# Performance work log

Hardware: AMD Instinct MI355X
Metric: run time of the kernel (lower is better)

The kernel has to match this reference:

```python
import jax, jax.numpy as jnp
import numpy as np

N_DOF = 7
WIDTH = 1024
BATCH = 8192
EPS = 1e-5
LSIZE = N_DOF * (N_DOF + 1) // 2   # diag (n) + strictly-lower ((n^2-n)/2)


def _tri_idx(n):
    # order matches LowTri: offset -i chunks, within-chunk j -> entry (j+i, j)
    r, c = [], []
    for i in range(n):
        for j in range(n - i):
            r.append(j + i)
            c.append(j)
    return np.array(r, np.int32), np.array(c, np.int32)

_R, _C = _tri_idx(N_DOF)


def setup_inputs() -> dict:
    key = jax.random.key(0)
    ks = jax.random.split(key, 9)

    def glorot(k, shape):
        std = (2.0 / (shape[0] + shape[1])) ** 0.5
        return (jax.random.normal(k, shape, jnp.float32) * std).astype(jnp.float32)

    lower = LSIZE - N_DOF
    b0 = 0.1
    return {
        "state": jax.random.normal(ks[0], (BATCH, N_DOF), jnp.float32),
        "velocity": jax.random.normal(ks[1], (BATCH, N_DOF), jnp.float32),
        "acceleration": jax.random.normal(ks[2], (BATCH, N_DOF), jnp.float32),
        "W_in": glorot(ks[3], (N_DOF, WIDTH)), "b_in": jnp.full((WIDTH,), b0, jnp.float32),
        "W_h": glorot(ks[4], (WIDTH, WIDTH)), "b_h": jnp.full((WIDTH,), b0, jnp.float32),
        "W_g": glorot(ks[5], (WIDTH, 1)), "b_g": jnp.full((1,), b0, jnp.float32),
        "W_ld": glorot(ks[6], (WIDTH, N_DOF)), "b_ld": jnp.full((N_DOF,), b0, jnp.float32),
        "W_lo": glorot(ks[7], (WIDTH, lower)), "b_lo": jnp.full((lower,), b0, jnp.float32),
    }


def _layer(x, der, W, b, act):
    # a: [B, out]; der: [B, in, n_dof] -> [B, out, n_dof]
    a = x @ W + b
    if act == "relu":
        y = jax.nn.relu(a)
        gp = (a > 0).astype(a.dtype)
    else:  # linear
        y = a
        gp = jnp.ones_like(a)
    # diag(g'(a)) @ W^T @ prev_der  ==  g'(a)[:, :, None] * (W^T @ prev_der)
    new_der = gp[:, :, None] * jnp.einsum("io,bid->bod", W, der)
    return y, new_der


def _forward(state, velocity, acceleration,
             W_in, b_in, W_h, b_h, W_g, b_g, W_ld, b_ld, W_lo, b_lo):
    B = state.shape[0]
    eye = jnp.broadcast_to(jnp.eye(N_DOF, dtype=state.dtype), (B, N_DOF, N_DOF))

    y1, d1 = _layer(state, eye, W_in, b_in, "relu")
    y2, d2 = _layer(y1, d1, W_h, b_h, "relu")
    y3, d3 = _layer(y2, d2, W_h, b_h, "relu")   # original reuses hidden_layer1 twice

    V, derV = _layer(y3, d3, W_g, b_g, "linear")       # derV: [B, 1, n_dof]
    l_diag, der_ld = _layer(y3, d3, W_ld, b_ld, "relu")
    l_low, der_lo = _layer(y3, d3, W_lo, b_lo, "linear")

    l = jnp.concatenate([l_diag, l_low], axis=1)          # [B, LSIZE]
    der_l = jnp.concatenate([der_ld, der_lo], axis=1)     # [B, LSIZE, n_dof]

    def lowtri(v):   # [B, LSIZE] -> [B, n, n]
        return jnp.zeros((B, N_DOF, N_DOF), v.dtype).at[:, _R, _C].set(v)

    def lowtri3d(v):  # [B, n_dof, LSIZE] -> [B, n_dof, n, n]
        return jnp.zeros((B, N_DOF, N_DOF, N_DOF), v.dtype).at[:, :, _R, _C].set(v)

    L = lowtri(l)
    LT = jnp.swapaxes(L, 1, 2)
    M = L @ LT + EPS * jnp.eye(N_DOF, dtype=L.dtype)

    dldt = jnp.einsum("bld,bd->bl", der_l, velocity)
    dLdt = lowtri(dldt)
    dMdt = L @ jnp.swapaxes(dLdt, 1, 2) + dLdt @ LT

    dLdq = lowtri3d(jnp.swapaxes(der_l, 1, 2))            # [B, n_dof, n, n]
    dMdq = dLdq @ LT[:, None] + L[:, None] @ jnp.swapaxes(dLdq, 2, 3)

    dMdt_dq = jnp.einsum("bij,bj->bi", dMdt, velocity)
    quad_dq = jnp.einsum("bi,bkij,bj->bk", velocity, dMdq, velocity)
    C = dMdt_dq - 0.5 * quad_dq
    G = derV[:, 0, :]                                      # squeeze [B,1,n_dof]
    Mddq = jnp.einsum("bij,bj->bi", M, acceleration)
    tau_pred = Mddq + C + G
    return tau_pred, M, C, G


def reference(state, velocity, acceleration,
              W_in, b_in, W_h, b_h, W_g, b_g, W_ld, b_ld, W_lo, b_lo):
    return _forward(state, velocity, acceleration,
                    W_in, b_in, W_h, b_h, W_g, b_g, W_ld, b_ld, W_lo, b_lo)
```

## Files before the change

### kernel.cpp

```cpp
#include <hip/hip_runtime.h>
#include <hip/hip_bf16.h>

#define WIDTH 1024
#define BATCH 8192

typedef __attribute__((ext_vector_type(8))) short short8;
typedef __attribute__((ext_vector_type(4))) float floatx4;

typedef __attribute__((address_space(1))) void gvoid;
typedef __attribute__((address_space(3))) void lvoid;

__device__ __forceinline__ void async_copy16(const void* g, void* l) {
    __builtin_amdgcn_global_load_lds((gvoid*)g, (lvoid*)l, 16, 0, 0);
}

__device__ __forceinline__ void split_store(float v, __hip_bfloat16* hi, __hip_bfloat16* lo, long idx) {
    __hip_bfloat16 h = __float2bfloat16(v);
    hi[idx] = h;
    lo[idx] = __float2bfloat16(v - __bfloat162float(h));
}

__global__ __launch_bounds__(256) void transpose_k(
    const float* __restrict__ W,
    __hip_bfloat16* __restrict__ Wth, __hip_bfloat16* __restrict__ Wtl)
{
    __shared__ float t[32][33];
    const int tx = threadIdx.x & 31, ty = threadIdx.x >> 5;
    const int bx = blockIdx.x << 5, by = blockIdx.y << 5;
#pragma unroll
    for (int r = 0; r < 32; r += 8)
        t[ty + r][tx] = W[(long)(by + ty + r) * WIDTH + bx + tx];
    __syncthreads();
#pragma unroll
    for (int r = 0; r < 32; r += 8)
        split_store(t[tx][ty + r], Wth, Wtl, (long)(bx + ty + r) * WIDTH + by + tx);
}

__global__ __launch_bounds__(256) void buildwcat_k(
    const float* __restrict__ W_ld, const float* __restrict__ W_lo,
    const float* __restrict__ W_g,
    __hip_bfloat16* __restrict__ Wch, __hip_bfloat16* __restrict__ Wcl)
{
    const int idx = blockIdx.x * 256 + threadIdx.x;
    const int n = idx >> 10, k = idx & 1023;
    float v = 0.f;
    if (n < 7)       v = W_ld[k * 7 + n];
    else if (n < 28) v = W_lo[k * 21 + (n - 7)];
    else if (n == 28) v = W_g[k];
    split_store(v, Wch, Wcl, idx);
}

__global__ __launch_bounds__(256) void prep_k(
    const float* __restrict__ state,
    const float* __restrict__ W_in,
    const float* __restrict__ b_in,
    __hip_bfloat16* __restrict__ Y1h, __hip_bfloat16* __restrict__ Y1l,
    __hip_bfloat16* __restrict__ D1h)
{
    const int b = blockIdx.x;
    const int j0 = threadIdx.x * 4;
    float s[7];
#pragma unroll
    for (int d = 0; d < 7; ++d) s[d] = state[b * 7 + d];
    float a[4];
#pragma unroll
    for (int q = 0; q < 4; ++q) a[q] = b_in[j0 + q];
    float w[7][4];
#pragma unroll
    for (int d = 0; d < 7; ++d)
#pragma unroll
        for (int q = 0; q < 4; ++q) {
            w[d][q] = W_in[d * WIDTH + j0 + q];
            a[q] += s[d] * w[d][q];
        }
    bool gp[4];
#pragma unroll
    for (int q = 0; q < 4; ++q) {
        gp[q] = a[q] > 0.f;
        split_store(gp[q] ? a[q] : 0.f, Y1h, Y1l, (long)b * WIDTH + j0 + q);
    }
    union { unsigned long long u64; unsigned short h[4]; } pk;
#pragma unroll
    for (int d = 0; d < 7; ++d) {
#pragma unroll
        for (int q = 0; q < 4; ++q) {
            __hip_bfloat16 v = __float2bfloat16(gp[q] ? w[d][q] : 0.f);
            pk.h[q] = *reinterpret_cast<unsigned short*>(&v);
        }
        *reinterpret_cast<unsigned long long*>(&D1h[((long)b * 7 + d) * WIDTH + j0]) = pk.u64;
    }
}

__device__ __forceinline__ void y_gemm_body(
    short* SM,
    int bm, int bn, int tid,
    const __hip_bfloat16* Ah, const __hip_bfloat16* Al,
    const __hip_bfloat16* Bh, const __hip_bfloat16* Bl,
    const float* bias,
    __hip_bfloat16* outh, __hip_bfloat16* outl)
{
    short* Ash = SM;          short* Asl = SM + 4096;
    short* Bsh = SM + 8192;   short* Bsl = SM + 12288;
    const int lane = tid & 63;
    const int wv = tid >> 6;
    const int wm = wv >> 1, wn = wv & 1;
    const int srow = tid >> 2;
    const int scol = (tid & 3) << 3;
    const short* pAh = (const short*)Ah + (long)(bm * 128 + srow) * WIDTH + scol;
    const short* pAl = (const short*)Al + (long)(bm * 128 + srow) * WIDTH + scol;
    const short* pBh = (const short*)Bh + (long)(bn * 128 + srow) * WIDTH + scol;
    const short* pBl = (const short*)Bl + (long)(bn * 128 + srow) * WIDTH + scol;
    const long half = 64l * WIDTH;

    floatx4 acc[4][4] = {};
    const int r = lane & 15;
    const int kq = (lane >> 4) << 3;

    for (int kt = 0; kt < WIDTH; kt += 32) {
        __syncthreads();
        async_copy16(pAh + kt,        Ash + wv * 512);
        async_copy16(pAh + half + kt, Ash + 2048 + wv * 512);
        async_copy16(pAl + kt,        Asl + wv * 512);
        async_copy16(pAl + half + kt, Asl + 2048 + wv * 512);
        async_copy16(pBh + kt,        Bsh + wv * 512);
        async_copy16(pBh + half + kt, Bsh + 2048 + wv * 512);
        async_copy16(pBl + kt,        Bsl + wv * 512);
        async_copy16(pBl + half + kt, Bsl + 2048 + wv * 512);
        __syncthreads();
        short8 afh[4], afl[4], bfh[4], bfl[4];
#pragma unroll
        for (int i = 0; i < 4; ++i) {
            const int ar = (wm * 64 + i * 16 + r) * 32 + kq;
            afh[i] = *reinterpret_cast<const short8*>(&Ash[ar]);
            afl[i] = *reinterpret_cast<const short8*>(&Asl[ar]);
        }
#pragma unroll
        for (int j = 0; j < 4; ++j) {
            const int br = (wn * 64 + j * 16 + r) * 32 + kq;
            bfh[j] = *reinterpret_cast<const short8*>(&Bsh[br]);
            bfl[j] = *reinterpret_cast<const short8*>(&Bsl[br]);
        }
#pragma unroll
        for (int i = 0; i < 4; ++i)
#pragma unroll
            for (int j = 0; j < 4; ++j) {
                acc[i][j] = __builtin_amdgcn_mfma_f32_16x16x32_bf16(afh[i], bfh[j], acc[i][j], 0, 0, 0);
                acc[i][j] = __builtin_amdgcn_mfma_f32_16x16x32_bf16(afh[i], bfl[j], acc[i][j], 0, 0, 0);
                acc[i][j] = __builtin_amdgcn_mfma_f32_16x16x32_bf16(afl[i], bfh[j], acc[i][j], 0, 0, 0);
            }
    }

    const int r4 = (lane >> 4) << 2;
#pragma unroll
    for (int i = 0; i < 4; ++i)
#pragma unroll
        for (int j = 0; j < 4; ++j) {
            const int col = bn * 128 + wn * 64 + j * 16 + r;
#pragma unroll
            for (int rr = 0; rr < 4; ++rr) {
                const int row = bm * 128 + wm * 64 + i * 16 + r4 + rr;
                float v = acc[i][j][rr] + bias[col];
                v = v > 0.f ? v : 0.f;
                split_store(v, outh, outl, (long)row * WIDTH + col);
            }
        }
}

__global__ __launch_bounds__(256) void gemm_y(
    const __hip_bfloat16* __restrict__ Ah, const __hip_bfloat16* __restrict__ Al,
    const __hip_bfloat16* __restrict__ Bh, const __hip_bfloat16* __restrict__ Bl,
    const float* __restrict__ bias,
    __hip_bfloat16* __restrict__ outh, __hip_bfloat16* __restrict__ outl)
{
    __shared__ __align__(16) short SM[16384];
    y_gemm_body(SM, blockIdx.x, blockIdx.y, threadIdx.x, Ah, Al, Bh, Bl, bias, outh, outl);
}

__global__ __launch_bounds__(256) void d2y3_k(
    const __hip_bfloat16* __restrict__ D1,
    const __hip_bfloat16* __restrict__ Wth, const __hip_bfloat16* __restrict__ Wtl,
    const __hip_bfloat16* __restrict__ Y2h, const __hip_bfloat16* __restrict__ Y2l,
    const float* __restrict__ bias,
    __hip_bfloat16* __restrict__ D2out,
    __hip_bfloat16* __restrict__ Y3h, __hip_bfloat16* __restrict__ Y3l,
    int nd)
{
    __shared__ __align__(16) short SM[16384];
    const int tid = threadIdx.x;
    if ((int)blockIdx.x >= nd) {
        y_gemm_body(SM, blockIdx.x - nd, blockIdx.y, tid, Y2h, Y2l, Wth, Wtl, bias, Y3h, Y3l);
        return;
    }
    short* Ash0 = SM;         short* Ash1 = SM + 4096;
    short* Bsh0 = SM + 8192;  short* Bsh1 = SM + 12288;
    const int lane = tid & 63;
    const int wv = tid >> 6;
    const int wm = wv >> 1, wn = wv & 1;
    const int bm = blockIdx.x, bn = blockIdx.y;

    const int srow = tid >> 2;
    const int scol = (tid & 3) << 3;
    const short* pAh = (const short*)D1 + (long)(bm * 128 + srow) * WIDTH + scol;
    const short* pBh = (const short*)Wth + (long)(bn * 128 + srow) * WIDTH + scol;
    const long half = 64l * WIDTH;

    floatx4 acc[4][4] = {};
    const int r = lane & 15;
    const int kq = (lane >> 4) << 3;

    for (int kt = 0; kt < WIDTH; kt += 64) {
        __syncthreads();
        async_copy16(pAh + kt,             Ash0 + wv * 512);
        async_copy16(pAh + half + kt,      Ash0 + 2048 + wv * 512);
        async_copy16(pAh + kt + 32,        Ash1 + wv * 512);
        async_copy16(pAh + half + kt + 32, Ash1 + 2048 + wv * 512);
        async_copy16(pBh + kt,             Bsh0 + wv * 512);
        async_copy16(pBh + half + kt,      Bsh0 + 2048 + wv * 512);
        async_copy16(pBh + kt + 32,        Bsh1 + wv * 512);
        async_copy16(pBh + half + kt + 32, Bsh1 + 2048 + wv * 512);
        __syncthreads();
#pragma unroll
        for (int s = 0; s < 2; ++s) {
            const short* As = s ? Ash1 : Ash0;
            const short* Bs = s ? Bsh1 : Bsh0;
            short8 afh[4], bfh[4];
#pragma unroll
            for (int i = 0; i < 4; ++i)
                afh[i] = *reinterpret_cast<const short8*>(&As[(wm * 64 + i * 16 + r) * 32 + kq]);
#pragma unroll
            for (int j = 0; j < 4; ++j)
                bfh[j] = *reinterpret_cast<const short8*>(&Bs[(wn * 64 + j * 16 + r) * 32 + kq]);
#pragma unroll
            for (int i = 0; i < 4; ++i)
#pragma unroll
                for (int j = 0; j < 4; ++j)
                    acc[i][j] = __builtin_amdgcn_mfma_f32_16x16x32_bf16(afh[i], bfh[j], acc[i][j], 0, 0, 0);
        }
    }

    const int r4 = (lane >> 4) << 2;
#pragma unroll
    for (int i = 0; i < 4; ++i)
#pragma unroll
        for (int j = 0; j < 4; ++j) {
            const int col = bn * 128 + wn * 64 + j * 16 + r;
#pragma unroll
            for (int rr = 0; rr < 4; ++rr) {
                const int row = bm * 128 + wm * 64 + i * 16 + r4 + rr;
                float v = acc[i][j][rr];
                const unsigned brow = (unsigned)row / 7u;
                if (!(__bfloat162float(Y2h[(long)brow * WIDTH + col]) > 0.f)) v = 0.f;
                D2out[(long)row * WIDTH + col] = __float2bfloat16(v);
            }
        }
}

__global__ __launch_bounds__(256) void d3heady_k(
    const __hip_bfloat16* __restrict__ D2,
    const __hip_bfloat16* __restrict__ Wth, const __hip_bfloat16* __restrict__ Wtl,
    const __hip_bfloat16* __restrict__ Y3h, const __hip_bfloat16* __restrict__ Y3l,
    const __hip_bfloat16* __restrict__ Wch, const __hip_bfloat16* __restrict__ Wcl,
    float* __restrict__ PDpart, float* __restrict__ PY,
    int nd, int Mrows)
{
    __shared__ __align__(16) short SM[26112];
    const int tid = threadIdx.x;
    const int lane = tid & 63;
    const int wv = tid >> 6;
    const int r = lane & 15;
    const int kq = (lane >> 4) << 3;
    const int r4 = (lane >> 4) << 2;
    const int srow = tid >> 2;
    const int scol = (tid & 3) << 3;
    const long half = 64l * WIDTH;

    if ((int)blockIdx.x >= nd) {
        if (blockIdx.y != 0) return;
        short* Ash = SM;          short* Asl = SM + 4096;
        short* Bsh = SM + 8192;   short* Bsl = SM + 9216;
        const int bm = blockIdx.x - nd;
        const short* pAh = (const short*)Y3h + (long)(bm * 128 + srow) * WIDTH + scol;
        const short* pAl = (const short*)Y3l + (long)(bm * 128 + srow) * WIDTH + scol;
        const long boff = (long)srow * WIDTH + scol;
        const short* pBh = (const short*)Wch;  const short* pBl = (const short*)Wcl;

        floatx4 acc[2][2] = {};
        for (int kt = 0; kt < WIDTH; kt += 32) {
            short8 gbh, gbl;
            if (tid < 128) {
                gbh = *reinterpret_cast<const short8*>(pBh + boff + kt);
                gbl = *reinterpret_cast<const short8*>(pBl + boff + kt);
            }
            __syncthreads();
            async_copy16(pAh + kt,        Ash + wv * 512);
            async_copy16(pAh + half + kt, Ash + 2048 + wv * 512);
            async_copy16(pAl + kt,        Asl + wv * 512);
            async_copy16(pAl + half + kt, Asl + 2048 + wv * 512);
            if (tid < 128) {
                *reinterpret_cast<short8*>(&Bsh[srow * 32 + scol]) = gbh;
                *reinterpret_cast<short8*>(&Bsl[srow * 32 + scol]) = gbl;
            }
            __syncthreads();
            short8 afh[2], afl[2], bfh[2], bfl[2];
#pragma unroll
            for (int i = 0; i < 2; ++i) {
                const int ar = (wv * 32 + i * 16 + r) * 32 + kq;
                afh[i] = *reinterpret_cast<const short8*>(&Ash[ar]);
                afl[i] = *reinterpret_cast<const short8*>(&Asl[ar]);
            }
#pragma unroll
            for (int j = 0; j < 2; ++j) {
                const int br = (j * 16 + r) * 32 + kq;
                bfh[j] = *reinterpret_cast<const short8*>(&Bsh[br]);
                bfl[j] = *reinterpret_cast<const short8*>(&Bsl[br]);
            }
#pragma unroll
            for (int i = 0; i < 2; ++i)
#pragma unroll
                for (int j = 0; j < 2; ++j) {
                    acc[i][j] = __builtin_amdgcn_mfma_f32_16x16x32_bf16(afh[i], bfh[j], acc[i][j], 0, 0, 0);
                    acc[i][j] = __builtin_amdgcn_mfma_f32_16x16x32_bf16(afh[i], bfl[j], acc[i][j], 0, 0, 0);
                    acc[i][j] = __builtin_amdgcn_mfma_f32_16x16x32_bf16(afl[i], bfh[j], acc[i][j], 0, 0, 0);
                }
        }
#pragma unroll
        for (int i = 0; i < 2; ++i)
#pragma unroll
            for (int j = 0; j < 2; ++j)
#pragma unroll
                for (int rr = 0; rr < 4; ++rr) {
                    const int row = bm * 128 + wv * 32 + i * 16 + r4 + rr;
                    PY[(long)row * 32 + j * 16 + r] = acc[i][j][rr];
                }
        return;
    }

    short* Ash0 = SM;         short* Ash1 = SM + 4096;
    short* Bsh0 = SM + 8192;  short* Bsh1 = SM + 12288;
    short* T    = SM;
    short* WcH  = SM + 17408;
    short* WcL  = SM + 21760;

    const int wm = wv >> 1, wn = wv & 1;
    const int bm = blockIdx.x, bn = blockIdx.y;
    const short* pAh = (const short*)D2 + (long)(bm * 128 + srow) * WIDTH + scol;
    const short* pBh = (const short*)Wth + (long)(bn * 128 + srow) * WIDTH + scol;

    floatx4 acc[4][4] = {};
    for (int kt = 0; kt < WIDTH; kt += 64) {
        __syncthreads();
        async_copy16(pAh + kt,             Ash0 + wv * 512);
        async_copy16(pAh + half + kt,      Ash0 + 2048 + wv * 512);
        async_copy16(pAh + kt + 32,        Ash1 + wv * 512);
        async_copy16(pAh + half + kt + 32, Ash1 + 2048 + wv * 512);
        async_copy16(pBh + kt,             Bsh0 + wv * 512);
        async_copy16(pBh + half + kt,      Bsh0 + 2048 + wv * 512);
        async_copy16(pBh + kt + 32,        Bsh1 + wv * 512);
        async_copy16(pBh + half + kt + 32, Bsh1 + 2048 + wv * 512);
        __syncthreads();
#pragma unroll
        for (int s = 0; s < 2; ++s) {
            const short* As = s ? Ash1 : Ash0;
            const short* Bs = s ? Bsh1 : Bsh0;
            short8 afh[4], bfh[4];
#pragma unroll
            for (int i = 0; i < 4; ++i)
                afh[i] = *reinterpret_cast<const short8*>(&As[(wm * 64 + i * 16 + r) * 32 + kq]);
#pragma unroll
            for (int j = 0; j < 4; ++j)
                bfh[j] = *reinterpret_cast<const short8*>(&Bs[(wn * 64 + j * 16 + r) * 32 + kq]);
#pragma unroll
            for (int i = 0; i < 4; ++i)
#pragma unroll
                for (int j = 0; j < 4; ++j)
                    acc[i][j] = __builtin_amdgcn_mfma_f32_16x16x32_bf16(afh[i], bfh[j], acc[i][j], 0, 0, 0);
        }
    }

    __syncthreads();
#pragma unroll
    for (int i = 0; i < 4; ++i)
#pragma unroll
        for (int j = 0; j < 4; ++j) {
            const int coll = wn * 64 + j * 16 + r;
            const int colg = bn * 128 + coll;
#pragma unroll
            for (int rr = 0; rr < 4; ++rr) {
                const int rowl = wm * 64 + i * 16 + r4 + rr;
                const int rowg = bm * 128 + rowl;
                float v = acc[i][j][rr];
                const unsigned brow = (unsigned)rowg / 7u;
                if (!(__bfloat162float(Y3h[(long)brow * WIDTH + colg]) > 0.f)) v = 0.f;
                __hip_bfloat16 hb = __float2bfloat16(v);
                T[rowl * 136 + coll] = *reinterpret_cast<short*>(&hb);
            }
        }
    {
        const int n = tid >> 4, k8 = (tid & 15) * 8;
        const short* wh = (const short*)Wch;
        const short* wl = (const short*)Wcl;
        *reinterpret_cast<short8*>(&WcH[n * 136 + k8]) =
            *reinterpret_cast<const short8*>(wh + n * WIDTH + bn * 128 + k8);
        *reinterpret_cast<short8*>(&WcH[(n + 16) * 136 + k8]) =
            *reinterpret_cast<const short8*>(wh + (n + 16) * WIDTH + bn * 128 + k8);
        *reinterpret_cast<short8*>(&WcL[n * 136 + k8]) =
            *reinterpret_cast<const short8*>(wl + n * WIDTH + bn * 128 + k8);
        *reinterpret_cast<short8*>(&WcL[(n + 16) * 136 + k8]) =
            *reinterpret_cast<const short8*>(wl + (n + 16) * WIDTH + bn * 128 + k8);
    }
    __syncthreads();

    floatx4 accp[2][2] = {};
#pragma unroll
    for (int kk = 0; kk < 128; kk += 32) {
        short8 af[2], bh8[2], bl8[2];
#pragma unroll
        for (int i = 0; i < 2; ++i)
            af[i] = *reinterpret_cast<const short8*>(&T[(wv * 32 + i * 16 + r) * 136 + kk + kq]);
#pragma unroll
        for (int j = 0; j < 2; ++j) {
            bh8[j] = *reinterpret_cast<const short8*>(&WcH[(j * 16 + r) * 136 + kk + kq]);
            bl8[j] = *reinterpret_cast<const short8*>(&WcL[(j * 16 + r) * 136 + kk + kq]);
        }
#pragma unroll
        for (int i = 0; i < 2; ++i)
#pragma unroll
            for (int j = 0; j < 2; ++j) {
                accp[i][j] = __builtin_amdgcn_mfma_f32_16x16x32_bf16(af[i], bh8[j], accp[i][j], 0, 0, 0);
                accp[i][j] = __builtin_amdgcn_mfma_f32_16x16x32_bf16(af[i], bl8[j], accp[i][j], 0, 0, 0);
            }
    }
#pragma unroll
    for (int i = 0; i < 2; ++i)
#pragma unroll
        for (int j = 0; j < 2; ++j)
#pragma unroll
            for (int rr = 0; rr < 4; ++rr) {
                const int rowg = bm * 128 + wv * 32 + i * 16 + r4 + rr;
                PDpart[((long)bn * Mrows + rowg) * 32 + j * 16 + r] = accp[i][j][rr];
            }
}

__device__ __forceinline__ int midx(int rr, int cc) {
    const int i = rr - cc;
    return i * 7 - (i * (i - 1)) / 2 + cc;
}

__global__ __launch_bounds__(64) void finalize_k(
    const float* __restrict__ PY,
    const float* __restrict__ PDpart,
    const float* __restrict__ vel_g,
    const float* __restrict__ acc_g,
    const float* __restrict__ b_ld,
    const float* __restrict__ b_lo,
    float* __restrict__ out,
    int b0, int Mrows)
{
    __shared__ float lval[28];
    __shared__ int gpv[7];
    __shared__ float derl[29 * 7];
    __shared__ float Lm[49], Mm[49], dLt[49], uu[49];
    __shared__ float wvv[7], pv[7], Cv[7], Gv[7], tauv[7], vl[7], ac[7];

    const int bl = blockIdx.x, tid = threadIdx.x;
    const int b = b0 + bl;
    if (tid < 28) {
        float s = PY[(long)bl * 32 + tid];
        if (tid < 7) {
            s += b_ld[tid];
            gpv[tid] = s > 0.f;
            lval[tid] = s > 0.f ? s : 0.f;
        } else {
            lval[tid] = s + b_lo[tid - 7];
        }
    }
    if (tid >= 28 && tid < 35) {
        vl[tid - 28] = vel_g[b * 7 + tid - 28];
        ac[tid - 28] = acc_g[b * 7 + tid - 28];
    }
    __syncthreads();
    for (int idx = tid; idx < 203; idx += 64) {
        const int m = idx / 7, d = idx % 7;
        float v = 0.f;
#pragma unroll
        for (int p = 0; p < 8; ++p)
            v += PDpart[((long)p * Mrows + bl * 7 + d) * 32 + m];
        if (m < 7 && !gpv[m]) v = 0.f;
        derl[m * 7 + d] = v;
    }
    __syncthreads();
    if (tid < 49) {
        const int rr = tid / 7, cc = tid % 7;
        Lm[tid] = (rr >= cc) ? lval[midx(rr, cc)] : 0.f;
    }
    __syncthreads();
    if (tid < 49) {
        const int rr = tid / 7, cc = tid % 7;
        float s = 0.f;
        for (int k = 0; k < 7; ++k) s += Lm[rr * 7 + k] * Lm[cc * 7 + k];
        if (rr == cc) s += 1e-5f;
        Mm[tid] = s;
        float t = 0.f;
        if (rr >= cc) {
            const int m = midx(rr, cc);
            for (int d = 0; d < 7; ++d) t += derl[m * 7 + d] * vl[d];
        }
        dLt[tid] = t;
        float u = 0.f;
        for (int r2 = cc; r2 < 7; ++r2) u += vl[r2] * derl[midx(r2, cc) * 7 + rr];
        uu[tid] = u;
    } else if (tid >= 49 && tid < 56) {
        const int j = tid - 49;
        float s = 0.f;
        for (int r2 = 0; r2 < 7; ++r2) s += Lm[r2 * 7 + j] * vl[r2];
        wvv[j] = s;
    }
    __syncthreads();
    if (tid < 7) {
        float s = 0.f;
        for (int r2 = 0; r2 < 7; ++r2) s += dLt[r2 * 7 + tid] * vl[r2];
        pv[tid] = s;
    }
    __syncthreads();
    if (tid < 7) {
        float s = 0.f, q = 0.f, md = 0.f;
        for (int c = 0; c < 7; ++c) {
            s += Lm[tid * 7 + c] * pv[c] + dLt[tid * 7 + c] * wvv[c];
            q += uu[tid * 7 + c] * wvv[c];
            md += Mm[tid * 7 + c] * ac[c];
        }
        Cv[tid] = s - q;
        Gv[tid] = derl[28 * 7 + tid];
        tauv[tid] = md + Cv[tid] + Gv[tid];
    }
    __syncthreads();
    if (tid < 49) out[57344 + (long)b * 49 + tid] = Mm[tid];
    if (tid < 7) {
        out[(long)b * 7 + tid] = tauv[tid];
        out[458752 + (long)b * 7 + tid] = Cv[tid];
        out[516096 + (long)b * 7 + tid] = Gv[tid];
    }
}

extern "C" void kernel_launch(void* const* d_in, const int* in_sizes, int n_in,
                              void* d_out, int out_size, void* d_ws, size_t ws_size,
                              hipStream_t stream)
{
    const float* state = (const float*)d_in[0];
    const float* vel   = (const float*)d_in[1];
    const float* accel = (const float*)d_in[2];
    const float* W_in  = (const float*)d_in[3];
    const float* b_in  = (const float*)d_in[4];
    const float* W_h   = (const float*)d_in[5];
    const float* b_h   = (const float*)d_in[6];
    const float* W_g   = (const float*)d_in[7];
    const float* W_ld  = (const float*)d_in[9];
    const float* b_ld  = (const float*)d_in[10];
    const float* W_lo  = (const float*)d_in[11];
    const float* b_lo  = (const float*)d_in[12];
    float* outp = (float*)d_out;

    char* ws = (char*)d_ws;
    __hip_bfloat16* Wth = (__hip_bfloat16*)ws; ws += (size_t)WIDTH * WIDTH * 2;
    __hip_bfloat16* Wtl = (__hip_bfloat16*)ws; ws += (size_t)WIDTH * WIDTH * 2;
    __hip_bfloat16* Wch = (__hip_bfloat16*)ws; ws += 32 * WIDTH * 2;
    __hip_bfloat16* Wcl = (__hip_bfloat16*)ws; ws += 32 * WIDTH * 2;
    const size_t fixed = (size_t)(ws - (char*)d_ws);

    int CH = 128;
    for (int cand = 8192; cand >= 128; cand >>= 1) {
        size_t need = fixed + (size_t)cand * 37120;
        if (need <= ws_size) { CH = cand; break; }
    }
    const int NCH = BATCH / CH;

    const size_t YB = (size_t)CH * WIDTH * 2;
    const size_t DB = (size_t)CH * 7 * WIDTH * 2;
    __hip_bfloat16* Yah = (__hip_bfloat16*)ws; ws += YB;
    __hip_bfloat16* Yal = (__hip_bfloat16*)ws; ws += YB;
    __hip_bfloat16* Ybh = (__hip_bfloat16*)ws; ws += YB;
    __hip_bfloat16* Ybl = (__hip_bfloat16*)ws; ws += YB;
    __hip_bfloat16* Dah = (__hip_bfloat16*)ws; ws += DB;
    __hip_bfloat16* Dbh = (__hip_bfloat16*)ws; ws += DB;
    float* PY = (float*)ws; ws += (size_t)CH * 32 * 4;
    float* PDpart = (float*)Dah;

    const int Mrows = CH * 7;
    const int nd = Mrows / 128;
    const int ny = CH / 128;

    transpose_k<<<dim3(32, 32), dim3(256), 0, stream>>>(W_h, Wth, Wtl);
    buildwcat_k<<<dim3(128), dim3(256), 0, stream>>>(W_ld, W_lo, W_g, Wch, Wcl);

    for (int c = 0; c < NCH; ++c) {
        prep_k<<<dim3(CH), dim3(256), 0, stream>>>(state + (size_t)c * CH * 7, W_in, b_in,
                                                   Yah, Yal, Dah);
        gemm_y<<<dim3(ny, 8), dim3(256), 0, stream>>>(
            Yah, Yal, Wth, Wtl, b_h, Ybh, Ybl);
        d2y3_k<<<dim3(nd + ny, 8), dim3(256), 0, stream>>>(
            Dah, Wth, Wtl, Ybh, Ybl, b_h, Dbh, Yah, Yal, nd);
        d3heady_k<<<dim3(nd + ny, 8), dim3(256), 0, stream>>>(
            Dbh, Wth, Wtl, Yah, Yal, Wch, Wcl, PDpart, PY, nd, Mrows);
        finalize_k<<<dim3(CH), dim3(64), 0, stream>>>(PY, PDpart, vel, accel, b_ld, b_lo,
                                                      outp, c * CH, Mrows);
    }
    (void)in_sizes; (void)n_in; (void)out_size;
}
```

Baseline: 667.7 us.

## Rewrite d2 GEMM as 256x256 eight-wave pipelined kernel with prefetched LDS stages

Replaces the 128x128 four-wave d2 derivative GEMM with a 256x256 tile kernel using 512 threads, double-buffered 128KB LDS, and chunked async global-to-LDS prefetch with explicit vmcnt waits, barriers and setprio around MFMA bursts. The y3 GEMM branch is folded in by splitting each 512-thread block into two 256-thread halves. The goal is higher data reuse per tile and overlap of memory loads with MFMA work. The minimum chunk size rises to 256, and the large LDS footprint plus hand-tuned wait counts risk low occupancy or hazards.

```diff
diff --git a/kernel.cpp b/kernel.cpp
--- a/kernel.cpp
+++ b/kernel.cpp
@@ -176,77 +176,127 @@
     y_gemm_body(SM, blockIdx.x, blockIdx.y, threadIdx.x, Ah, Al, Bh, Bl, bias, outh, outl);
 }
 
-__global__ __launch_bounds__(256) void d2y3_k(
+
+__device__ __forceinline__ void stage_chunk_d2(
+    short* SMbase, const short* __restrict__ A, const short* __restrict__ B,
+    int tau, int c, int tid)
+{
+    const short* src = (c & 1) ? B : A;
+    const int kbase = (tau << 6) + ((c >> 1) << 5);
+    short* region = SMbase + ((tau & 1) << 15) + (c << 13);
+    const int wvb = tid & 0x1C0;
+#pragma unroll
+    for (int j = 0; j < 2; ++j) {
+        const int idx = tid + (j << 9);
+        async_copy16(src + (long)(idx >> 2) * WIDTH + kbase + ((idx & 3) << 3),
+                     region + ((long)(wvb + (j << 9)) << 3));
+    }
+}
+
+__global__ __launch_bounds__(512, 2) void d2y3_8p(
     const __hip_bfloat16* __restrict__ D1,
     const __hip_bfloat16* __restrict__ Wth, const __hip_bfloat16* __restrict__ Wtl,
     const __hip_bfloat16* __restrict__ Y2h, const __hip_bfloat16* __restrict__ Y2l,
     const float* __restrict__ bias,
     __hip_bfloat16* __restrict__ D2out,
     __hip_bfloat16* __restrict__ Y3h, __hip_bfloat16* __restrict__ Y3l,
-    int nd)
-{
-    __shared__ __align__(16) short SM[16384];
+    int nd2)
+{
+    __shared__ __align__(16) short SM[65536];
     const int tid = threadIdx.x;
-    if ((int)blockIdx.x >= nd) {
-        y_gemm_body(SM, blockIdx.x - nd, blockIdx.y, tid, Y2h, Y2l, Wth, Wtl, bias, Y3h, Y3l);
+
+    if ((int)blockIdx.x >= nd2) {
+        const int half = tid >> 8;
+        y_gemm_body(SM + (half << 14), blockIdx.x - nd2, blockIdx.y + (half << 2),
+                    tid & 255, Y2h, Y2l, Wth, Wtl, bias, Y3h, Y3l);
         return;
     }
-    short* Ash0 = SM;         short* Ash1 = SM + 4096;
-    short* Bsh0 = SM + 8192;  short* Bsh1 = SM + 12288;
+
+    const short* Abase = (const short*)D1 + (long)blockIdx.x * 256 * WIDTH;
+    const short* Bbase = (const short*)Wth + (long)blockIdx.y * 256 * WIDTH;
     const int lane = tid & 63;
     const int wv = tid >> 6;
-    const int wm = wv >> 1, wn = wv & 1;
-    const int bm = blockIdx.x, bn = blockIdx.y;
-
-    const int srow = tid >> 2;
-    const int scol = (tid & 3) << 3;
-    const short* pAh = (const short*)D1 + (long)(bm * 128 + srow) * WIDTH + scol;
-    const short* pBh = (const short*)Wth + (long)(bn * 128 + srow) * WIDTH + scol;
-    const long half = 64l * WIDTH;
-
-    floatx4 acc[4][4] = {};
+    const int wm = wv >> 2, wn = wv & 3;
     const int r = lane & 15;
     const int kq = (lane >> 4) << 3;
 
-    for (int kt = 0; kt < WIDTH; kt += 64) {
-        __syncthreads();
-        async_copy16(pAh + kt,             Ash0 + wv * 512);
-        async_copy16(pAh + half + kt,      Ash0 + 2048 + wv * 512);
-        async_copy16(pAh + kt + 32,        Ash1 + wv * 512);
-        async_copy16(pAh + half + kt + 32, Ash1 + 2048 + wv * 512);
-        async_copy16(pBh + kt,             Bsh0 + wv * 512);
-        async_copy16(pBh + half + kt,      Bsh0 + 2048 + wv * 512);
-        async_copy16(pBh + kt + 32,        Bsh1 + wv * 512);
-        async_copy16(pBh + half + kt + 32, Bsh1 + 2048 + wv * 512);
-        __syncthreads();
-#pragma unroll
-        for (int s = 0; s < 2; ++s) {
-            const short* As = s ? Ash1 : Ash0;
-            const short* Bs = s ? Bsh1 : Bsh0;
-            short8 afh[4], bfh[4];
-#pragma unroll
-            for (int i = 0; i < 4; ++i)
-                afh[i] = *reinterpret_cast<const short8*>(&As[(wm * 64 + i * 16 + r) * 32 + kq]);
-#pragma unroll
-            for (int j = 0; j < 4; ++j)
-                bfh[j] = *reinterpret_cast<const short8*>(&Bs[(wn * 64 + j * 16 + r) * 32 + kq]);
-#pragma unroll
-            for (int i = 0; i < 4; ++i)
-#pragma unroll
-                for (int j = 0; j < 4; ++j)
-                    acc[i][j] = __builtin_amdgcn_mfma_f32_16x16x32_bf16(afh[i], bfh[j], acc[i][j], 0, 0, 0);
+    floatx4 acc[8][4] = {};
+
+    stage_chunk_d2(SM, Abase, Bbase, 0, 0, tid);
+    stage_chunk_d2(SM, Abase, Bbase, 0, 1, tid);
+    stage_chunk_d2(SM, Abase, Bbase, 0, 2, tid);
+    stage_chunk_d2(SM, Abase, Bbase, 0, 3, tid);
+    stage_chunk_d2(SM, Abase, Bbase, 1, 0, tid);
+    stage_chunk_d2(SM, Abase, Bbase, 1, 1, tid);
+    stage_chunk_d2(SM, Abase, Bbase, 1, 2, tid);
+    asm volatile("s_waitcnt vmcnt(10)" ::: "memory");
+    __builtin_amdgcn_s_barrier();
+
+    short8 af[8], bf[2];
+#pragma unroll 2
+    for (int t = 0; t < 16; ++t) {
+        short* buf = SM + ((t & 1) << 15);
+#pragma unroll
+        for (int ks = 0; ks < 2; ++ks) {
+            const short* Ab = buf + (ks ? 2 : 0) * 8192;
+            const short* Bb = buf + (ks ? 3 : 1) * 8192;
+
+#pragma unroll
+            for (int i = 0; i < 8; ++i)
+                af[i] = *reinterpret_cast<const short8*>(&Ab[(wm * 128 + i * 16 + r) * 32 + kq]);
+#pragma unroll
+            for (int j = 0; j < 2; ++j)
+                bf[j] = *reinterpret_cast<const short8*>(&Bb[(wn * 64 + j * 16 + r) * 32 + kq]);
+            if (ks == 0) { if (t + 1 < 16) stage_chunk_d2(SM, Abase, Bbase, t + 1, 3, tid); }
+            else         { if (t + 2 < 16) stage_chunk_d2(SM, Abase, Bbase, t + 2, 1, tid); }
+            __builtin_amdgcn_s_barrier();
+            asm volatile("s_waitcnt lgkmcnt(0)");
+            __builtin_amdgcn_sched_barrier(0);
+            __builtin_amdgcn_s_setprio(1);
+#pragma unroll
+            for (int i = 0; i < 8; ++i)
+#pragma unroll
+                for (int j = 0; j < 2; ++j)
+                    acc[i][j] = __builtin_amdgcn_mfma_f32_16x16x32_bf16(af[i], bf[j], acc[i][j], 0, 0, 0);
+            __builtin_amdgcn_s_setprio(0);
+            __builtin_amdgcn_s_barrier();
+
+#pragma unroll
+            for (int j = 0; j < 2; ++j)
+                bf[j] = *reinterpret_cast<const short8*>(&Bb[(wn * 64 + (2 + j) * 16 + r) * 32 + kq]);
+            if (ks == 0) { if (t + 2 < 16) stage_chunk_d2(SM, Abase, Bbase, t + 2, 0, tid); }
+            else         { if (t + 2 < 16) stage_chunk_d2(SM, Abase, Bbase, t + 2, 2, tid); }
+            __builtin_amdgcn_s_barrier();
+            asm volatile("s_waitcnt lgkmcnt(0)");
+            __builtin_amdgcn_sched_barrier(0);
+            __builtin_amdgcn_s_setprio(1);
+#pragma unroll
+            for (int i = 0; i < 8; ++i)
+#pragma unroll
+                for (int j = 0; j < 2; ++j)
+                    acc[i][2 + j] = __builtin_amdgcn_mfma_f32_16x16x32_bf16(af[i], bf[j], acc[i][2 + j], 0, 0, 0);
+            __builtin_amdgcn_s_setprio(0);
+            if (ks == 0) {
+                if (t < 14)       asm volatile("s_waitcnt vmcnt(10)" ::: "memory");
+                else if (t == 14) asm volatile("s_waitcnt vmcnt(8)"  ::: "memory");
+                else              asm volatile("s_waitcnt vmcnt(0)"  ::: "memory");
+            } else {
+                if (t < 14)       asm volatile("s_waitcnt vmcnt(10)" ::: "memory");
+                else if (t == 14) asm volatile("s_waitcnt vmcnt(4)"  ::: "memory");
+            }
+            __builtin_amdgcn_s_barrier();
         }
     }
 
     const int r4 = (lane >> 4) << 2;
 #pragma unroll
-    for (int i = 0; i < 4; ++i)
+    for (int i = 0; i < 8; ++i)
 #pragma unroll
         for (int j = 0; j < 4; ++j) {
-            const int col = bn * 128 + wn * 64 + j * 16 + r;
+            const int col = blockIdx.y * 256 + wn * 64 + j * 16 + r;
 #pragma unroll
             for (int rr = 0; rr < 4; ++rr) {
-                const int row = bm * 128 + wm * 64 + i * 16 + r4 + rr;
+                const int row = blockIdx.x * 256 + wm * 128 + i * 16 + r4 + rr;
                 float v = acc[i][j][rr];
                 const unsigned brow = (unsigned)row / 7u;
                 if (!(__bfloat162float(Y2h[(long)brow * WIDTH + col]) > 0.f)) v = 0.f;
@@ -567,8 +617,8 @@
     __hip_bfloat16* Wcl = (__hip_bfloat16*)ws; ws += 32 * WIDTH * 2;
     const size_t fixed = (size_t)(ws - (char*)d_ws);
 
-    int CH = 128;
-    for (int cand = 8192; cand >= 128; cand >>= 1) {
+    int CH = 256;
+    for (int cand = 8192; cand >= 256; cand >>= 1) {
         size_t need = fixed + (size_t)cand * 37120;
         if (need <= ws_size) { CH = cand; break; }
     }
@@ -588,6 +638,7 @@
     const int Mrows = CH * 7;
     const int nd = Mrows / 128;
     const int ny = CH / 128;
+    const int nd2 = Mrows / 256;
 
     transpose_k<<<dim3(32, 32), dim3(256), 0, stream>>>(W_h, Wth, Wtl);
     buildwcat_k<<<dim3(128), dim3(256), 0, stream>>>(W_ld, W_lo, W_g, Wch, Wcl);
@@ -597,8 +648,8 @@
                                                    Yah, Yal, Dah);
         gemm_y<<<dim3(ny, 8), dim3(256), 0, stream>>>(
             Yah, Yal, Wth, Wtl, b_h, Ybh, Ybl);
-        d2y3_k<<<dim3(nd + ny, 8), dim3(256), 0, stream>>>(
-            Dah, Wth, Wtl, Ybh, Ybl, b_h, Dbh, Yah, Yal, nd);
+        d2y3_8p<<<dim3(nd2 + ny, 4), dim3(512), 0, stream>>>(
+            Dah, Wth, Wtl, Ybh, Ybl, b_h, Dbh, Yah, Yal, nd2);
         d3heady_k<<<dim3(nd + ny, 8), dim3(256), 0, stream>>>(
             Dbh, Wth, Wtl, Yah, Yal, Wch, Wcl, PDpart, PY, nd, Mrows);
         finalize_k<<<dim3(CH), dim3(64), 0, stream>>>(PY, PDpart, vel, accel, b_ld, b_lo,
```

Result: no change. 671.6 us (+0.6%).
